# Kernel optimization log

Measured on AMD Instinct MI355X. Metric: run time of the kernel, lower is better.

Reference implementation:

```python
import jax, jax.numpy as jnp
import numpy as np

L, B, N, D, H, DH, M = 2, 8, 1024, 256, 4, 64, 512
EPS = 1e-5


def setup_inputs() -> dict:
    key = jax.random.key(0)
    ks = jax.random.split(key, 24)
    n = lambda k, shape, s=0.02: jax.random.normal(k, shape, dtype=jnp.float32) * s
    return {
        "x": jax.random.normal(ks[0], (B, N, D), dtype=jnp.float32),
        "ln1_g": jnp.ones((L, D), jnp.float32), "ln1_b": jnp.zeros((L, D), jnp.float32),
        "w_qkv": n(ks[1], (L, D, 3 * H * DH)),
        "w_out": n(ks[2], (L, H * DH, D)), "b_out": jnp.zeros((L, D), jnp.float32),
        "ln2_g": jnp.ones((L, D), jnp.float32), "ln2_b": jnp.zeros((L, D), jnp.float32),
        "w_fc1": n(ks[3], (L, D, M)), "b_fc1": jnp.zeros((L, M), jnp.float32),
        "wh": n(ks[4], (L, M, 3), 0.3), "bh": jnp.zeros((L, M), jnp.float32),
        "wv": n(ks[5], (L, M, 3), 0.3), "bv": jnp.zeros((L, M), jnp.float32),
        "bn_g": jnp.ones((L, M), jnp.float32), "bn_b": jnp.zeros((L, M), jnp.float32),
        "bn_m": n(ks[6], (L, M), 0.1),
        "bn_v": jax.random.uniform(ks[7], (L, M), jnp.float32, 0.5, 1.5),
        "w_fc2": n(ks[8], (L, M, D)), "b_fc2": jnp.zeros((L, D), jnp.float32),
        "ls_w1": n(ks[9], (L, D, D // 4)), "ls_w2": n(ks[10], (L, D // 4, D)),
    }


def _ln(z, g, b):
    mu = z.mean(-1, keepdims=True)
    var = ((z - mu) ** 2).mean(-1, keepdims=True)
    return (z - mu) / jnp.sqrt(var + EPS) * g + b


def _lsrc(z, w1, w2):
    # SE gate: global mean over tokens -> FC -> ReLU -> FC -> sigmoid -> scale
    s = jax.nn.sigmoid(jax.nn.relu(z.mean(1) @ w1) @ w2)  # [B, D]
    return z * s[:, None, :]


def reference(x, ln1_g, ln1_b, w_qkv, w_out, b_out, ln2_g, ln2_b, w_fc1, b_fc1,
              wh, bh, wv, bv, bn_g, bn_b, bn_m, bn_v, w_fc2, b_fc2, ls_w1, ls_w2):
    scale = DH ** -0.5
    for l in range(L):
        # --- MHSA (pre-LN) ---
        h = _ln(x, ln1_g[l], ln1_b[l])
        qkv = h @ w_qkv[l]                                  # [B,N,3*H*DH]
        q, k, v = jnp.split(qkv, 3, axis=-1)
        split = lambda t: t.reshape(B, N, H, DH).transpose(0, 2, 1, 3)  # [B,H,N,DH]
        q, k, v = split(q), split(k), split(v)
        attn = jax.nn.softmax(jnp.einsum('bhid,bhjd->bhij', q, k) * scale, axis=-1)
        o = jnp.einsum('bhij,bhjd->bhid', attn, v)
        o = o.transpose(0, 2, 1, 3).reshape(B, N, H * DH)
        y = o @ w_out[l] + b_out[l]                          # dropout = identity (eval)
        x = _lsrc(x + y, ls_w1[l], ls_w2[l])
        # --- MLP with ACB depthwise conv over the token axis ---
        y = jax.nn.gelu(_ln(x, ln2_g[l], ln2_b[l]) @ w_fc1[l] + b_fc1[l], approximate=False)
        # conv_h: depthwise 1x3 conv along N (zero pad)
        yp = jnp.pad(y, ((0, 0), (1, 1), (0, 0)))
        ch = wh[l, :, 0] * yp[:, :-2] + wh[l, :, 1] * yp[:, 1:-1] + wh[l, :, 2] * yp[:, 2:] + bh[l]
        # conv_v: 3x1 depthwise conv on height-1 input with pad 1 -> only center tap
        cv = wv[l, :, 1] * y + bv[l]
        z = ch + cv
        z = (z - bn_m[l]) / jnp.sqrt(bn_v[l] + EPS) * bn_g[l] + bn_b[l]  # BN (eval)
        z = jax.nn.gelu(z, approximate=False)
        y = z @ w_fc2[l] + b_fc2[l]
        x = _lsrc(x + y, ls_w1[l], ls_w2[l])
    return x
```

## Files before the change

### kernel.cpp

```cpp
#include <hip/hip_runtime.h>
#include <hip/hip_bf16.h>
#include <math.h>

#define EPSF 1e-5f

typedef short bf16x8 __attribute__((ext_vector_type(8)));
typedef float f32x4  __attribute__((ext_vector_type(4)));

#define S_BARRIER   __asm__ volatile("s_barrier" ::: "memory")
#define S_WAITV(n)  __asm__ volatile("s_waitcnt vmcnt(" #n ")" ::: "memory")
#define S_WAITL0    __asm__ volatile("s_waitcnt lgkmcnt(0)" ::: "memory")

__device__ __forceinline__ float gelu_f(float z){
  return 0.5f*z*(1.0f + erff(z*0.70710678118654752f));
}
__device__ __forceinline__ unsigned short f2bf(float f){
  unsigned u = __float_as_uint(f);
  u += 0x7FFFu + ((u >> 16) & 1u);
  return (unsigned short)(u >> 16);
}
__device__ __forceinline__ float bf2f(unsigned short u){
  return __uint_as_float((unsigned)u << 16);
}
__device__ __forceinline__ void gll16(const unsigned short* g, unsigned short* l){
  __builtin_amdgcn_global_load_lds(
    (const __attribute__((address_space(1))) unsigned int*)g,
    (__attribute__((address_space(3))) unsigned int*)l, 16, 0, 0);
}

__global__ void tcast_all_k(const float* __restrict__ wqkv, const float* __restrict__ wout,
                            const float* __restrict__ wfc1, const float* __restrict__ wfc2,
                            unsigned short* __restrict__ oqkv, unsigned short* __restrict__ oout,
                            unsigned short* __restrict__ ofc1, unsigned short* __restrict__ ofc2,
                            const float* __restrict__ wh, const float* __restrict__ bh,
                            const float* __restrict__ wv, const float* __restrict__ bv,
                            const float* __restrict__ g, const float* __restrict__ bb,
                            const float* __restrict__ mm, const float* __restrict__ vv,
                            float* __restrict__ cp){
  int idx = blockIdx.x*256 + threadIdx.x;
  if (idx < 1048576){
    int l = idx >> 19; int r = idx & 524287;
    const float* in; unsigned short* out; int K, N, base;
    if (r < 196608)      { in=wqkv+ (long)l*196608; out=oqkv+(long)l*196608; K=256; N=768; base=r; }
    else if (r < 262144) { in=wout+ (long)l*65536;  out=oout+(long)l*65536;  K=256; N=256; base=r-196608; }
    else if (r < 393216) { in=wfc1+ (long)l*131072; out=ofc1+(long)l*131072; K=256; N=512; base=r-262144; }
    else                 { in=wfc2+ (long)l*131072; out=ofc2+(long)l*131072; K=512; N=256; base=r-393216; }
    int n = base / K, k = base % K;
    out[base] = f2bf(in[(long)k*N + n]);
  } else if (idx < 1048576 + 1024){
    int j2 = idx - 1048576;
    int l = j2 >> 9, j = j2 & 511;
    int o = l*512 + j;
    float sc = g[o]*rsqrtf(vv[o] + EPSF);
    float* c = cp + (long)l*6*512;
    c[0*512+j] = wh[o*3+0];
    c[1*512+j] = wh[o*3+1] + wv[o*3+1];
    c[2*512+j] = wh[o*3+2];
    c[3*512+j] = bh[o] + bv[o];
    c[4*512+j] = sc;
    c[5*512+j] = bb[o] - mm[o]*sc;
  }
}

__global__ void ln_bf_k(const float* __restrict__ x, const float* __restrict__ g,
                        const float* __restrict__ b, unsigned short* __restrict__ out){
  const int row = blockIdx.x;
  const int t = threadIdx.x;
  float v = x[(long)row*256 + t];
  float s = v, s2 = v*v;
  for (int o=32;o>0;o>>=1){ s += __shfl_down(s,o); s2 += __shfl_down(s2,o); }
  __shared__ float ls[4], ls2[4];
  const int w = t>>6, lane = t&63;
  if (lane==0){ ls[w]=s; ls2[w]=s2; }
  __syncthreads();
  if (t==0){
    float a  = ls[0]+ls[1]+ls[2]+ls[3];
    float a2 = ls2[0]+ls2[1]+ls2[2]+ls2[3];
    float mu = a*(1.f/256.f);
    float var = a2*(1.f/256.f) - mu*mu;
    ls[0]=mu; ls2[0]=rsqrtf(var+EPSF);
  }
  __syncthreads();
  out[(long)row*256+t] = f2bf((v-ls[0])*ls2[0]*g[t] + b[t]);
}

__global__ void seapply_ln_k(float* __restrict__ x, const float* __restrict__ gate,
                             const float* __restrict__ g, const float* __restrict__ b,
                             unsigned short* __restrict__ out){
  const int row = blockIdx.x;
  const int t = threadIdx.x;
  const int bi = row >> 10;
  float v = x[(long)row*256 + t] * gate[bi*256 + t];
  x[(long)row*256 + t] = v;
  float s = v, s2 = v*v;
  for (int o=32;o>0;o>>=1){ s += __shfl_down(s,o); s2 += __shfl_down(s2,o); }
  __shared__ float ls[4], ls2[4];
  const int w = t>>6, lane = t&63;
  if (lane==0){ ls[w]=s; ls2[w]=s2; }
  __syncthreads();
  if (t==0){
    float a  = ls[0]+ls[1]+ls[2]+ls[3];
    float a2 = ls2[0]+ls2[1]+ls2[2]+ls2[3];
    float mu = a*(1.f/256.f);
    float var = a2*(1.f/256.f) - mu*mu;
    ls[0]=mu; ls2[0]=rsqrtf(var+EPSF);
  }
  __syncthreads();
  out[(long)row*256+t] = f2bf((v-ls[0])*ls2[0]*g[t] + b[t]);
}

__global__ void seapply_out_k(const float* __restrict__ x, const float* __restrict__ gate,
                              float* __restrict__ o){
  long o4 = ((long)blockIdx.x*256 + threadIdx.x)*4;
  float4 v = *reinterpret_cast<const float4*>(x+o4);
  float4 g = *reinterpret_cast<const float4*>(gate + (((o4>>18)<<8) | (o4 & 255)));
  v.x*=g.x; v.y*=g.y; v.z*=g.z; v.w*=g.w;
  *reinterpret_cast<float4*>(o+o4) = v;
}

template<int ACT, bool RES, bool BIAS, int OUT, int BNT, bool CS>
__global__ __launch_bounds__(256,2)
void gmm_k(const unsigned short* __restrict__ A,
           const unsigned short* __restrict__ Bt,
           void* __restrict__ Cv, int ldc,
           const float* __restrict__ bias,
           const float* __restrict__ res,
           int K, unsigned short* __restrict__ vtb,
           float* __restrict__ cm)
{
  __shared__ unsigned short As[2][128*64];
  __shared__ unsigned short Bs[2][BNT*64];
  float* C = (float*)Cv;
  unsigned short* Cb = (unsigned short*)Cv;
  const int tid  = threadIdx.x;
  const int wave = tid>>6, lane = tid&63;
  constexpr int NJ = (BNT==128) ? 4 : 2;
  const int wm = (wave>>1)*64, wn = (wave&1)*(BNT/2);
  const int m0 = blockIdx.y*128, n0 = blockIdx.x*BNT;
  const int lrow = lane&15, quad = lane>>4;

  f32x4 acc[4][NJ];
  #pragma unroll
  for (int i=0;i<4;i++)
    #pragma unroll
    for (int j=0;j<NJ;j++)
      #pragma unroll
      for (int r=0;r<4;r++) acc[i][j][r]=0.f;

  auto stage = [&](int kt, int buf){
    const int k0 = kt<<6;
    #pragma unroll
    for (int it2=0; it2<4; it2++){
      int idx = tid + it2*256;
      int row = idx>>3, c = idx&7;
      gll16(A + (long)(m0+row)*K + k0 + c*8, &As[buf][idx*8]);
    }
    #pragma unroll
    for (int it2=0; it2<BNT/32; it2++){
      int idx = tid + it2*256;
      int row = idx>>3, c = idx&7;
      gll16(Bt + (long)(n0+row)*K + k0 + c*8, &Bs[buf][idx*8]);
    }
  };

  const int iters = K >> 6;
  stage(0, 0);

  for (int it=0; it<iters; it++){
    const int cur = it & 1;
    if (it+1 < iters){
      stage(it+1, cur^1);
      if (BNT==128) { S_WAITV(8); } else { S_WAITV(6); }
    } else {
      S_WAITV(0);
    }
    S_BARRIER;

    #pragma unroll
    for (int s=0;s<2;s++){
      bf16x8 a[4], b[NJ];
      const int ck = s*4 + quad;
      #pragma unroll
      for (int i=0;i<4;i++)
        a[i] = *reinterpret_cast<const bf16x8*>(&As[cur][(wm+16*i+lrow)*64 + ck*8]);
      #pragma unroll
      for (int j=0;j<NJ;j++)
        b[j] = *reinterpret_cast<const bf16x8*>(&Bs[cur][(wn+16*j+lrow)*64 + ck*8]);
      #pragma unroll
      for (int i=0;i<4;i++)
        #pragma unroll
        for (int j=0;j<NJ;j++)
          acc[i][j] = __builtin_amdgcn_mfma_f32_16x16x32_bf16(a[i], b[j], acc[i][j], 0,0,0);
    }
    S_WAITL0;
    S_BARRIER;
  }

  if (OUT==2 && n0 >= 512){
    unsigned short* lt = (unsigned short*)&As[0][0];
    #pragma unroll
    for (int i=0;i<4;i++){
      const int row_l0 = wm + 16*i + quad*4;
      #pragma unroll
      for (int j=0;j<NJ;j++){
        const int col_l = wn + 16*j + lrow;
        #pragma unroll
        for (int r=0;r<4;r++){
          const int row_l = row_l0 + r;
          lt[col_l*128 + (((row_l>>3) ^ (col_l&7))<<3) + (row_l&7)] = f2bf(acc[i][j][r]);
        }
      }
    }
    __syncthreads();
    const int bb = m0 >> 10, nn0 = m0 & 1023;
    #pragma unroll
    for (int it2=0; it2<8; it2++){
      int idx = tid + it2*256;
      int col_l = idx >> 4;
      int row8 = (idx & 15) << 3;
      uint4 v = *reinterpret_cast<const uint4*>(&lt[col_l*128 + (((row8>>3) ^ (col_l&7))<<3)]);
      int col = n0 + col_l;
      int h = (col-512) >> 6, d = (col-512) & 63;
      *reinterpret_cast<uint4*>(&vtb[(long)((bb*4+h)*64 + d)*1024 + nn0 + row8]) = v;
    }
    return;
  }

  float csum[NJ];
  #pragma unroll
  for (int j=0;j<NJ;j++) csum[j] = 0.f;

  #pragma unroll
  for (int i=0;i<4;i++){
    const int row0 = m0 + wm + 16*i + quad*4;
    #pragma unroll
    for (int j=0;j<NJ;j++){
      const int col = n0 + wn + 16*j + lrow;
      if (OUT==2){
        #pragma unroll
        for (int r=0;r<4;r++)
          Cb[(long)(row0+r)*512 + col] = f2bf(acc[i][j][r]);
      } else {
        const float bv = BIAS ? bias[col] : 0.f;
        #pragma unroll
        for (int r=0;r<4;r++){
          const long off = (long)(row0+r)*ldc + col;
          float v = acc[i][j][r] + bv;
          if (RES) v += res[off];
          if (ACT==1) v = gelu_f(v);
          if (CS) csum[j] += v;
          if (OUT==1) Cb[off] = f2bf(v); else C[off] = v;
        }
      }
    }
  }
  if (CS){
    float* red = (float*)&As[0][0];
    for (int j = tid; j < BNT; j += 256) red[j] = 0.f;
    __syncthreads();
    #pragma unroll
    for (int j=0;j<NJ;j++)
      atomicAdd(&red[wn + 16*j + lrow], csum[j]);
    __syncthreads();
    const int bb = m0 >> 10;
    for (int j = tid; j < BNT; j += 256)
      atomicAdd(&cm[bb*256 + n0 + j], red[j]);
  }
}

__global__ __launch_bounds__(256)
void attn_k(const unsigned short* __restrict__ qkb,
            const unsigned short* __restrict__ vtb,
            unsigned short* __restrict__ op, float* __restrict__ ml){
  const int q0 = blockIdx.x * 64;
  const int bh = blockIdx.y;
  const int kz = blockIdx.z;
  const int b = bh >> 2, h = bh & 3;
  const int tid = threadIdx.x;
  const int wv = tid >> 6;
  const int lane = tid & 63;
  const int l15 = lane & 15, quad = lane >> 4;

  __shared__ unsigned short Qs[64*64];
  __shared__ unsigned short Ks[64*64];
  __shared__ unsigned short Vt[64*64];
  __shared__ unsigned short Ps[64*64];

  const long rowbase = (long)b*1024;
  const unsigned short* vsrc = vtb + (long)bh*64*1024;

  for (int f = tid; f < 512; f += 256){
    int row = f >> 3, g = f & 7;
    *reinterpret_cast<uint4*>(&Qs[row*64 + (g ^ (row&7))*8]) =
      *reinterpret_cast<const uint4*>(qkb + (rowbase + q0 + row)*512 + h*64 + g*8);
  }

  float lp[4];
  f32x4 acc[4];
  #pragma unroll
  for (int r=0;r<4;r++) lp[r] = 0.f;
  #pragma unroll
  for (int j=0;j<4;j++)
    #pragma unroll
    for (int r=0;r<4;r++) acc[j][r] = 0.f;

  const int kbeg = kz*512, kend = kbeg + 512;
  for (int k0 = kbeg; k0 < kend; k0 += 64){
    __syncthreads();
    for (int f = tid; f < 512; f += 256){
      int row = f >> 3, g = f & 7;
      *reinterpret_cast<uint4*>(&Ks[row*64 + (g ^ (row&7))*8]) =
        *reinterpret_cast<const uint4*>(qkb + (rowbase + k0 + row)*512 + 256 + h*64 + g*8);
      *reinterpret_cast<uint4*>(&Vt[row*64 + (g ^ (row&7))*8]) =
        *reinterpret_cast<const uint4*>(vsrc + (long)row*1024 + k0 + g*8);
    }
    __syncthreads();

    f32x4 s[4];
    #pragma unroll
    for (int j=0;j<4;j++)
      #pragma unroll
      for (int r=0;r<4;r++) s[j][r] = 0.f;

    #pragma unroll
    for (int half=0; half<2; half++){
      const int ck = half*4 + quad;
      const int qrow = 16*wv + l15;
      bf16x8 a = *reinterpret_cast<const bf16x8*>(&Qs[qrow*64 + (ck ^ (qrow&7))*8]);
      #pragma unroll
      for (int j=0;j<4;j++){
        int krow = 16*j + l15;
        bf16x8 bb = *reinterpret_cast<const bf16x8*>(&Ks[krow*64 + (ck ^ (krow&7))*8]);
        s[j] = __builtin_amdgcn_mfma_f32_16x16x32_bf16(a, bb, s[j], 0,0,0);
      }
    }

    #pragma unroll
    for (int r=0;r<4;r++)
      #pragma unroll
      for (int j=0;j<4;j++){
        float p = __expf(s[j][r]*0.125f);
        s[j][r] = p;
        lp[r] += p;
      }

    #pragma unroll
    for (int j=0;j<4;j++)
      #pragma unroll
      for (int r=0;r<4;r++){
        int rowq = 16*wv + quad*4 + r;
        int key = l15 + 16*j;
        Ps[rowq*64 + (((key>>3) ^ ((rowq>>2)&7)))*8 + (key&7)] = f2bf(s[j][r]);
      }

    #pragma unroll
    for (int half=0; half<2; half++){
      const int ck = half*4 + quad;
      const int prow = 16*wv + l15;
      bf16x8 a = *reinterpret_cast<const bf16x8*>(&Ps[prow*64 + (ck ^ ((prow>>2)&7))*8]);
      #pragma unroll
      for (int jj=0;jj<4;jj++){
        int drow = 16*jj + l15;
        bf16x8 bb = *reinterpret_cast<const bf16x8*>(&Vt[drow*64 + (ck ^ (drow&7))*8]);
        acc[jj] = __builtin_amdgcn_mfma_f32_16x16x32_bf16(a, bb, acc[jj], 0,0,0);
      }
    }
  }

  #pragma unroll
  for (int r=0;r<4;r++){
    float l = lp[r];
    l += __shfl_xor(l, 1); l += __shfl_xor(l, 2);
    l += __shfl_xor(l, 4); l += __shfl_xor(l, 8);
    const int rloc = q0 + 16*wv + quad*4 + r;
    const long grow = rowbase + rloc;
    #pragma unroll
    for (int jj=0;jj<4;jj++)
      op[((long)kz*8192 + grow)*256 + h*64 + 16*jj + l15] = f2bf(acc[jj][r]);
    if (l15 == 0)
      ml[((long)kz*32 + bh)*1024 + rloc] = l;
  }
}

__global__ void attn_merge_k(const unsigned short* __restrict__ op, const float* __restrict__ ml,
                             unsigned short* __restrict__ o, float* __restrict__ cm){
  if (blockIdx.x == 0){
    for (int i = threadIdx.x; i < 2048; i += 256) cm[i] = 0.f;
  }
  long off = ((long)blockIdx.x*256 + threadIdx.x)*4;
  int row = (int)(off >> 8);
  int col = (int)(off & 255);
  int h = col >> 6;
  int b = row >> 10, n = row & 1023;
  int bh = b*4 + h;
  float l0 = ml[(long)bh*1024 + n];
  float l1 = ml[32768 + (long)bh*1024 + n];
  float inv = 1.f / (l0 + l1);
  ushort4 a0 = *reinterpret_cast<const ushort4*>(op + off);
  ushort4 a1 = *reinterpret_cast<const ushort4*>(op + 2097152 + off);
  ushort4 u;
  u.x = f2bf((bf2f(a0.x) + bf2f(a1.x))*inv);
  u.y = f2bf((bf2f(a0.y) + bf2f(a1.y))*inv);
  u.z = f2bf((bf2f(a0.z) + bf2f(a1.z))*inv);
  u.w = f2bf((bf2f(a0.w) + bf2f(a1.w))*inv);
  *reinterpret_cast<ushort4*>(o + off) = u;
}

__global__ void segate2_k(const float* __restrict__ cm, const float* __restrict__ w1,
                          const float* __restrict__ w2, float* __restrict__ gate){
  const int b = blockIdx.x, t = threadIdx.x;
  __shared__ float sc[256], sh[64];
  sc[t] = cm[b*256+t]*(1.f/1024.f);
  __syncthreads();
  if (t < 64){
    float a=0.f;
    for (int k=0;k<256;k++) a += sc[k]*w1[k*64+t];
    sh[t] = fmaxf(a, 0.f);
  }
  __syncthreads();
  float a=0.f;
  for (int k=0;k<64;k++) a += sh[k]*w2[k*256+t];
  gate[b*256+t] = 1.f/(1.f+__expf(-a));
}

__global__ void conv_bf_k(const unsigned short* __restrict__ y, unsigned short* __restrict__ z,
                          const float* __restrict__ cp, float* __restrict__ cm)
{
  if (blockIdx.x == 0){
    for (int i = threadIdx.x; i < 2048; i += 256) cm[i] = 0.f;
  }
  const int t = threadIdx.x;
  const int rr = t >> 6;
  const int row = blockIdx.x*4 + rr;
  const int n = row & 1023;
  const int c8 = (t & 63) * 8;
  const long base = (long)row*512 + c8;

  uint4 uc = *reinterpret_cast<const uint4*>(y + base);
  uint4 um = (n>0)    ? *reinterpret_cast<const uint4*>(y + base - 512) : uint4{0,0,0,0};
  uint4 up = (n<1023) ? *reinterpret_cast<const uint4*>(y + base + 512) : uint4{0,0,0,0};
  const unsigned short* yc = reinterpret_cast<const unsigned short*>(&uc);
  const unsigned short* ym = reinterpret_cast<const unsigned short*>(&um);
  const unsigned short* yp = reinterpret_cast<const unsigned short*>(&up);

  float c0[8], c1[8], c2[8], c3[8], s5[8], b5[8];
  #pragma unroll
  for (int q=0;q<8;q+=4){
    *reinterpret_cast<float4*>(&c0[q]) = *reinterpret_cast<const float4*>(cp + 0*512 + c8 + q);
    *reinterpret_cast<float4*>(&c1[q]) = *reinterpret_cast<const float4*>(cp + 1*512 + c8 + q);
    *reinterpret_cast<float4*>(&c2[q]) = *reinterpret_cast<const float4*>(cp + 2*512 + c8 + q);
    *reinterpret_cast<float4*>(&c3[q]) = *reinterpret_cast<const float4*>(cp + 3*512 + c8 + q);
    *reinterpret_cast<float4*>(&s5[q]) = *reinterpret_cast<const float4*>(cp + 4*512 + c8 + q);
    *reinterpret_cast<float4*>(&b5[q]) = *reinterpret_cast<const float4*>(cp + 5*512 + c8 + q);
  }

  unsigned short outv[8];
  #pragma unroll
  for (int q=0;q<8;q++){
    float zz = c0[q]*bf2f(ym[q]) + c1[q]*bf2f(yc[q]) + c2[q]*bf2f(yp[q]) + c3[q];
    zz = zz*s5[q] + b5[q];
    outv[q] = f2bf(gelu_f(zz));
  }
  *reinterpret_cast<uint4*>(z + base) = *reinterpret_cast<uint4*>(outv);
}

extern "C" void kernel_launch(void* const* d_in, const int* in_sizes, int n_in,
                              void* d_out, int out_size, void* d_ws, size_t ws_size,
                              hipStream_t stream)
{
  const float* x_in  = (const float*)d_in[0];
  const float* ln1_g = (const float*)d_in[1];
  const float* ln1_b = (const float*)d_in[2];
  const float* w_qkv = (const float*)d_in[3];
  const float* w_out = (const float*)d_in[4];
  const float* b_out = (const float*)d_in[5];
  const float* ln2_g = (const float*)d_in[6];
  const float* ln2_b = (const float*)d_in[7];
  const float* w_fc1 = (const float*)d_in[8];
  const float* b_fc1 = (const float*)d_in[9];
  const float* wh    = (const float*)d_in[10];
  const float* bh    = (const float*)d_in[11];
  const float* wv    = (const float*)d_in[12];
  const float* bv    = (const float*)d_in[13];
  const float* bn_g  = (const float*)d_in[14];
  const float* bn_b  = (const float*)d_in[15];
  const float* bn_m  = (const float*)d_in[16];
  const float* bn_v  = (const float*)d_in[17];
  const float* w_fc2 = (const float*)d_in[18];
  const float* b_fc2 = (const float*)d_in[19];
  const float* ls_w1 = (const float*)d_in[20];
  const float* ls_w2 = (const float*)d_in[21];

  float* ws   = (float*)d_ws;
  float* xbuf = ws;
  float* mlb  = xbuf + 2097152;
  float* cm   = mlb + 65536;
  float* gate = cm + 2048;
  float* cpar = gate + 2048;
  unsigned short* habf = (unsigned short*)(cpar + 6144);
  unsigned short* opbf = habf + 2097152;
  unsigned short* qkb  = opbf + 4194304;
  unsigned short* vtb  = qkb  + 4194304;
  unsigned short* ybf  = vtb  + 2097152;
  unsigned short* zbf  = ybf  + 4194304;
  unsigned short* wqkv_t = zbf + 4194304;
  unsigned short* wout_t = wqkv_t + 393216;
  unsigned short* wfc1_t = wout_t + 131072;
  unsigned short* wfc2_t = wfc1_t + 262144;

  tcast_all_k<<<4100,256,0,stream>>>(w_qkv, w_out, w_fc1, w_fc2,
                                     wqkv_t, wout_t, wfc1_t, wfc2_t,
                                     wh, bh, wv, bv, bn_g, bn_b, bn_m, bn_v, cpar);

  for (int l=0;l<2;l++){
    const float* bout_l = b_out + l*256;
    const float* bfc1_l = b_fc1 + l*512;
    const float* bfc2_l = b_fc2 + l*256;
    const float* lw1_l  = ls_w1 + (long)l*256*64;
    const float* lw2_l  = ls_w2 + (long)l*64*256;
    const float* resx   = (l==0) ? x_in : xbuf;

    if (l==0)
      ln_bf_k<<<8192,256,0,stream>>>(x_in, ln1_g, ln1_b, habf);
    gmm_k<0,false,false,2,128,false><<<dim3(6,64),256,0,stream>>>(
        habf, wqkv_t + (long)l*768*256, (void*)qkb, 512, nullptr, nullptr, 256, vtb, nullptr);
    attn_k<<<dim3(16,32,2),256,0,stream>>>(qkb, vtb, opbf, mlb);
    attn_merge_k<<<2048,256,0,stream>>>(opbf, mlb, habf, cm);
    gmm_k<0,true,true,0,64,true><<<dim3(4,64),256,0,stream>>>(
        habf, wout_t + (long)l*256*256, (void*)xbuf, 256, bout_l, resx, 256, nullptr, cm);

    segate2_k<<<8,256,0,stream>>>(cm, lw1_l, lw2_l, gate);
    seapply_ln_k<<<8192,256,0,stream>>>(xbuf, gate, ln2_g + l*256, ln2_b + l*256, habf);

    gmm_k<1,false,true,1,128,false><<<dim3(4,64),256,0,stream>>>(
        habf, wfc1_t + (long)l*512*256, (void*)ybf, 512, bfc1_l, nullptr, 256, nullptr, nullptr);
    conv_bf_k<<<2048,256,0,stream>>>(ybf, zbf, cpar + (long)l*6*512, cm);
    gmm_k<0,true,true,0,64,true><<<dim3(4,64),256,0,stream>>>(
        zbf, wfc2_t + (long)l*256*512, (void*)xbuf, 256, bfc2_l, xbuf, 512, nullptr, cm);

    segate2_k<<<8,256,0,stream>>>(cm, lw1_l, lw2_l, gate);
    if (l==0)
      seapply_ln_k<<<8192,256,0,stream>>>(xbuf, gate, ln1_g + 256, ln1_b + 256, habf);
    else
      seapply_out_k<<<2048,256,0,stream>>>(xbuf, gate, (float*)d_out);
  }
}
```

Measured before the change: 336.4 us.

## Use one-wave-per-row LayerNorm, smaller M tiles for N=256 GEMMs, prefetch attention K/V

LayerNorm kernels now give each row to one wave with float4 loads and shuffle-only reductions, replacing the per-block shared-memory reduction and two barriers. The GEMM gains a BMT template parameter, and the out-projection and fc2 GEMMs use 64x64 tiles, doubling the grid to fill more CUs. The attention kernel prefetches the next K/V tile into registers while computing on the current one, which adds registers in exchange for hiding global load latency.

```diff
diff --git a/kernel.cpp b/kernel.cpp
--- a/kernel.cpp
+++ b/kernel.cpp
@@ -64,49 +64,51 @@
 
 __global__ void ln_bf_k(const float* __restrict__ x, const float* __restrict__ g,
                         const float* __restrict__ b, unsigned short* __restrict__ out){
-  const int row = blockIdx.x;
-  const int t = threadIdx.x;
-  float v = x[(long)row*256 + t];
-  float s = v, s2 = v*v;
-  for (int o=32;o>0;o>>=1){ s += __shfl_down(s,o); s2 += __shfl_down(s2,o); }
-  __shared__ float ls[4], ls2[4];
-  const int w = t>>6, lane = t&63;
-  if (lane==0){ ls[w]=s; ls2[w]=s2; }
-  __syncthreads();
-  if (t==0){
-    float a  = ls[0]+ls[1]+ls[2]+ls[3];
-    float a2 = ls2[0]+ls2[1]+ls2[2]+ls2[3];
-    float mu = a*(1.f/256.f);
-    float var = a2*(1.f/256.f) - mu*mu;
-    ls[0]=mu; ls2[0]=rsqrtf(var+EPSF);
-  }
-  __syncthreads();
-  out[(long)row*256+t] = f2bf((v-ls[0])*ls2[0]*g[t] + b[t]);
+  const int wv = threadIdx.x >> 6, lane = threadIdx.x & 63;
+  const int row = blockIdx.x*4 + wv;
+  const int c4 = lane*4;
+  float4 v = *reinterpret_cast<const float4*>(x + (long)row*256 + c4);
+  float s  = v.x+v.y+v.z+v.w;
+  float s2 = v.x*v.x+v.y*v.y+v.z*v.z+v.w*v.w;
+  #pragma unroll
+  for (int o=32;o>0;o>>=1){ s += __shfl_xor(s,o); s2 += __shfl_xor(s2,o); }
+  const float mu = s*(1.f/256.f);
+  const float rstd = rsqrtf(s2*(1.f/256.f) - mu*mu + EPSF);
+  float4 gg = *reinterpret_cast<const float4*>(g + c4);
+  float4 bb = *reinterpret_cast<const float4*>(b + c4);
+  ushort4 u;
+  u.x = f2bf((v.x-mu)*rstd*gg.x + bb.x);
+  u.y = f2bf((v.y-mu)*rstd*gg.y + bb.y);
+  u.z = f2bf((v.z-mu)*rstd*gg.z + bb.z);
+  u.w = f2bf((v.w-mu)*rstd*gg.w + bb.w);
+  *reinterpret_cast<ushort4*>(out + (long)row*256 + c4) = u;
 }
 
 __global__ void seapply_ln_k(float* __restrict__ x, const float* __restrict__ gate,
                              const float* __restrict__ g, const float* __restrict__ b,
                              unsigned short* __restrict__ out){
-  const int row = blockIdx.x;
-  const int t = threadIdx.x;
+  const int wv = threadIdx.x >> 6, lane = threadIdx.x & 63;
+  const int row = blockIdx.x*4 + wv;
   const int bi = row >> 10;
-  float v = x[(long)row*256 + t] * gate[bi*256 + t];
-  x[(long)row*256 + t] = v;
-  float s = v, s2 = v*v;
-  for (int o=32;o>0;o>>=1){ s += __shfl_down(s,o); s2 += __shfl_down(s2,o); }
-  __shared__ float ls[4], ls2[4];
-  const int w = t>>6, lane = t&63;
-  if (lane==0){ ls[w]=s; ls2[w]=s2; }
-  __syncthreads();
-  if (t==0){
-    float a  = ls[0]+ls[1]+ls[2]+ls[3];
-    float a2 = ls2[0]+ls2[1]+ls2[2]+ls2[3];
-    float mu = a*(1.f/256.f);
-    float var = a2*(1.f/256.f) - mu*mu;
-    ls[0]=mu; ls2[0]=rsqrtf(var+EPSF);
-  }
-  __syncthreads();
-  out[(long)row*256+t] = f2bf((v-ls[0])*ls2[0]*g[t] + b[t]);
+  const int c4 = lane*4;
+  float4 v = *reinterpret_cast<const float4*>(x + (long)row*256 + c4);
+  float4 gt = *reinterpret_cast<const float4*>(gate + bi*256 + c4);
+  v.x*=gt.x; v.y*=gt.y; v.z*=gt.z; v.w*=gt.w;
+  *reinterpret_cast<float4*>(x + (long)row*256 + c4) = v;
+  float s  = v.x+v.y+v.z+v.w;
+  float s2 = v.x*v.x+v.y*v.y+v.z*v.z+v.w*v.w;
+  #pragma unroll
+  for (int o=32;o>0;o>>=1){ s += __shfl_xor(s,o); s2 += __shfl_xor(s2,o); }
+  const float mu = s*(1.f/256.f);
+  const float rstd = rsqrtf(s2*(1.f/256.f) - mu*mu + EPSF);
+  float4 gg = *reinterpret_cast<const float4*>(g + c4);
+  float4 bb = *reinterpret_cast<const float4*>(b + c4);
+  ushort4 u;
+  u.x = f2bf((v.x-mu)*rstd*gg.x + bb.x);
+  u.y = f2bf((v.y-mu)*rstd*gg.y + bb.y);
+  u.z = f2bf((v.z-mu)*rstd*gg.z + bb.z);
+  u.w = f2bf((v.w-mu)*rstd*gg.w + bb.w);
+  *reinterpret_cast<ushort4*>(out + (long)row*256 + c4) = u;
 }
 
 __global__ void seapply_out_k(const float* __restrict__ x, const float* __restrict__ gate,
@@ -118,7 +120,7 @@
   *reinterpret_cast<float4*>(o+o4) = v;
 }
 
-template<int ACT, bool RES, bool BIAS, int OUT, int BNT, bool CS>
+template<int ACT, bool RES, bool BIAS, int OUT, int BMT, int BNT, bool CS>
 __global__ __launch_bounds__(256,2)
 void gmm_k(const unsigned short* __restrict__ A,
            const unsigned short* __restrict__ Bt,
@@ -128,20 +130,22 @@
            int K, unsigned short* __restrict__ vtb,
            float* __restrict__ cm)
 {
-  __shared__ unsigned short As[2][128*64];
+  __shared__ unsigned short As[2][BMT*64];
   __shared__ unsigned short Bs[2][BNT*64];
   float* C = (float*)Cv;
   unsigned short* Cb = (unsigned short*)Cv;
   const int tid  = threadIdx.x;
   const int wave = tid>>6, lane = tid&63;
-  constexpr int NJ = (BNT==128) ? 4 : 2;
-  const int wm = (wave>>1)*64, wn = (wave&1)*(BNT/2);
-  const int m0 = blockIdx.y*128, n0 = blockIdx.x*BNT;
+  constexpr int NI = BMT/32;
+  constexpr int NJ = BNT/32;
+  constexpr int NDMA = BMT/32 + BNT/32;
+  const int wm = (wave>>1)*(16*NI), wn = (wave&1)*(BNT/2);
+  const int m0 = blockIdx.y*BMT, n0 = blockIdx.x*BNT;
   const int lrow = lane&15, quad = lane>>4;
 
-  f32x4 acc[4][NJ];
-  #pragma unroll
-  for (int i=0;i<4;i++)
+  f32x4 acc[NI][NJ];
+  #pragma unroll
+  for (int i=0;i<NI;i++)
     #pragma unroll
     for (int j=0;j<NJ;j++)
       #pragma unroll
@@ -150,7 +154,7 @@
   auto stage = [&](int kt, int buf){
     const int k0 = kt<<6;
     #pragma unroll
-    for (int it2=0; it2<4; it2++){
+    for (int it2=0; it2<BMT/32; it2++){
       int idx = tid + it2*256;
       int row = idx>>3, c = idx&7;
       gll16(A + (long)(m0+row)*K + k0 + c*8, &As[buf][idx*8]);
@@ -170,7 +174,9 @@
     const int cur = it & 1;
     if (it+1 < iters){
       stage(it+1, cur^1);
-      if (BNT==128) { S_WAITV(8); } else { S_WAITV(6); }
+      if constexpr (NDMA==8) { S_WAITV(8); }
+      else if constexpr (NDMA==6) { S_WAITV(6); }
+      else { S_WAITV(4); }
     } else {
       S_WAITV(0);
     }
@@ -178,16 +184,16 @@
 
     #pragma unroll
     for (int s=0;s<2;s++){
-      bf16x8 a[4], b[NJ];
+      bf16x8 a[NI], b[NJ];
       const int ck = s*4 + quad;
       #pragma unroll
-      for (int i=0;i<4;i++)
+      for (int i=0;i<NI;i++)
         a[i] = *reinterpret_cast<const bf16x8*>(&As[cur][(wm+16*i+lrow)*64 + ck*8]);
       #pragma unroll
       for (int j=0;j<NJ;j++)
         b[j] = *reinterpret_cast<const bf16x8*>(&Bs[cur][(wn+16*j+lrow)*64 + ck*8]);
       #pragma unroll
-      for (int i=0;i<4;i++)
+      for (int i=0;i<NI;i++)
         #pragma unroll
         for (int j=0;j<NJ;j++)
           acc[i][j] = __builtin_amdgcn_mfma_f32_16x16x32_bf16(a[i], b[j], acc[i][j], 0,0,0);
@@ -196,61 +202,69 @@
     S_BARRIER;
   }
 
-  if (OUT==2 && n0 >= 512){
-    unsigned short* lt = (unsigned short*)&As[0][0];
-    #pragma unroll
-    for (int i=0;i<4;i++){
-      const int row_l0 = wm + 16*i + quad*4;
+  if constexpr (OUT==2){
+    if (n0 >= 512){
+      unsigned short* lt = (unsigned short*)&As[0][0];
+      #pragma unroll
+      for (int i=0;i<NI;i++){
+        const int row_l0 = wm + 16*i + quad*4;
+        #pragma unroll
+        for (int j=0;j<NJ;j++){
+          const int col_l = wn + 16*j + lrow;
+          #pragma unroll
+          for (int r=0;r<4;r++){
+            const int row_l = row_l0 + r;
+            lt[col_l*128 + (((row_l>>3) ^ (col_l&7))<<3) + (row_l&7)] = f2bf(acc[i][j][r]);
+          }
+        }
+      }
+      __syncthreads();
+      const int bb = m0 >> 10, nn0 = m0 & 1023;
+      #pragma unroll
+      for (int it2=0; it2<8; it2++){
+        int idx = tid + it2*256;
+        int col_l = idx >> 4;
+        int row8 = (idx & 15) << 3;
+        uint4 v = *reinterpret_cast<const uint4*>(&lt[col_l*128 + (((row8>>3) ^ (col_l&7))<<3)]);
+        int col = n0 + col_l;
+        int h = (col-512) >> 6, d = (col-512) & 63;
+        *reinterpret_cast<uint4*>(&vtb[(long)((bb*4+h)*64 + d)*1024 + nn0 + row8]) = v;
+      }
+      return;
+    }
+    #pragma unroll
+    for (int i=0;i<NI;i++){
+      const int row0 = m0 + wm + 16*i + quad*4;
       #pragma unroll
       for (int j=0;j<NJ;j++){
-        const int col_l = wn + 16*j + lrow;
-        #pragma unroll
-        for (int r=0;r<4;r++){
-          const int row_l = row_l0 + r;
-          lt[col_l*128 + (((row_l>>3) ^ (col_l&7))<<3) + (row_l&7)] = f2bf(acc[i][j][r]);
-        }
-      }
-    }
-    __syncthreads();
-    const int bb = m0 >> 10, nn0 = m0 & 1023;
-    #pragma unroll
-    for (int it2=0; it2<8; it2++){
-      int idx = tid + it2*256;
-      int col_l = idx >> 4;
-      int row8 = (idx & 15) << 3;
-      uint4 v = *reinterpret_cast<const uint4*>(&lt[col_l*128 + (((row8>>3) ^ (col_l&7))<<3)]);
-      int col = n0 + col_l;
-      int h = (col-512) >> 6, d = (col-512) & 63;
-      *reinterpret_cast<uint4*>(&vtb[(long)((bb*4+h)*64 + d)*1024 + nn0 + row8]) = v;
-    }
-    return;
-  }
-
-  float csum[NJ];
-  #pragma unroll
-  for (int j=0;j<NJ;j++) csum[j] = 0.f;
-
-  #pragma unroll
-  for (int i=0;i<4;i++){
-    const int row0 = m0 + wm + 16*i + quad*4;
-    #pragma unroll
-    for (int j=0;j<NJ;j++){
-      const int col = n0 + wn + 16*j + lrow;
-      if (OUT==2){
+        const int col = n0 + wn + 16*j + lrow;
         #pragma unroll
         for (int r=0;r<4;r++)
           Cb[(long)(row0+r)*512 + col] = f2bf(acc[i][j][r]);
-      } else {
-        const float bv = BIAS ? bias[col] : 0.f;
-        #pragma unroll
-        for (int r=0;r<4;r++){
-          const long off = (long)(row0+r)*ldc + col;
-          float v = acc[i][j][r] + bv;
-          if (RES) v += res[off];
-          if (ACT==1) v = gelu_f(v);
-          if (CS) csum[j] += v;
-          if (OUT==1) Cb[off] = f2bf(v); else C[off] = v;
-        }
+      }
+    }
+    return;
+  }
+
+  float csum[NJ];
+  #pragma unroll
+  for (int j=0;j<NJ;j++) csum[j] = 0.f;
+
+  #pragma unroll
+  for (int i=0;i<NI;i++){
+    const int row0 = m0 + wm + 16*i + quad*4;
+    #pragma unroll
+    for (int j=0;j<NJ;j++){
+      const int col = n0 + wn + 16*j + lrow;
+      const float bv = BIAS ? bias[col] : 0.f;
+      #pragma unroll
+      for (int r=0;r<4;r++){
+        const long off = (long)(row0+r)*ldc + col;
+        float v = acc[i][j][r] + bv;
+        if (RES) v += res[off];
+        if (ACT==1) v = gelu_f(v);
+        if (CS) csum[j] += v;
+        if (OUT==1) Cb[off] = f2bf(v); else C[off] = v;
       }
     }
   }
@@ -295,6 +309,16 @@
       *reinterpret_cast<const uint4*>(qkb + (rowbase + q0 + row)*512 + h*64 + g*8);
   }
 
+  const int row0 = tid >> 3, g0 = tid & 7;
+  const int row1 = row0 + 32;
+  uint4 kr0, vr0, kr1, vr1;
+  auto pre = [&](int k0){
+    kr0 = *reinterpret_cast<const uint4*>(qkb + (rowbase + k0 + row0)*512 + 256 + h*64 + g0*8);
+    vr0 = *reinterpret_cast<const uint4*>(vsrc + (long)row0*1024 + k0 + g0*8);
+    kr1 = *reinterpret_cast<const uint4*>(qkb + (rowbase + k0 + row1)*512 + 256 + h*64 + g0*8);
+    vr1 = *reinterpret_cast<const uint4*>(vsrc + (long)row1*1024 + k0 + g0*8);
+  };
+
   float lp[4];
   f32x4 acc[4];
   #pragma unroll
@@ -305,16 +329,14 @@
     for (int r=0;r<4;r++) acc[j][r] = 0.f;
 
   const int kbeg = kz*512, kend = kbeg + 512;
+  pre(kbeg);
   for (int k0 = kbeg; k0 < kend; k0 += 64){
+    *reinterpret_cast<uint4*>(&Ks[row0*64 + (g0 ^ (row0&7))*8]) = kr0;
+    *reinterpret_cast<uint4*>(&Vt[row0*64 + (g0 ^ (row0&7))*8]) = vr0;
+    *reinterpret_cast<uint4*>(&Ks[row1*64 + (g0 ^ (row1&7))*8]) = kr1;
+    *reinterpret_cast<uint4*>(&Vt[row1*64 + (g0 ^ (row1&7))*8]) = vr1;
     __syncthreads();
-    for (int f = tid; f < 512; f += 256){
-      int row = f >> 3, g = f & 7;
-      *reinterpret_cast<uint4*>(&Ks[row*64 + (g ^ (row&7))*8]) =
-        *reinterpret_cast<const uint4*>(qkb + (rowbase + k0 + row)*512 + 256 + h*64 + g*8);
-      *reinterpret_cast<uint4*>(&Vt[row*64 + (g ^ (row&7))*8]) =
-        *reinterpret_cast<const uint4*>(vsrc + (long)row*1024 + k0 + g*8);
-    }
-    __syncthreads();
+    if (k0 + 64 < kend) pre(k0 + 64);
 
     f32x4 s[4];
     #pragma unroll
@@ -365,6 +387,7 @@
         acc[jj] = __builtin_amdgcn_mfma_f32_16x16x32_bf16(a, bb, acc[jj], 0,0,0);
       }
     }
+    __syncthreads();
   }
 
   #pragma unroll
@@ -521,26 +544,26 @@
     const float* resx   = (l==0) ? x_in : xbuf;
 
     if (l==0)
-      ln_bf_k<<<8192,256,0,stream>>>(x_in, ln1_g, ln1_b, habf);
-    gmm_k<0,false,false,2,128,false><<<dim3(6,64),256,0,stream>>>(
+      ln_bf_k<<<2048,256,0,stream>>>(x_in, ln1_g, ln1_b, habf);
+    gmm_k<0,false,false,2,128,128,false><<<dim3(6,64),256,0,stream>>>(
         habf, wqkv_t + (long)l*768*256, (void*)qkb, 512, nullptr, nullptr, 256, vtb, nullptr);
     attn_k<<<dim3(16,32,2),256,0,stream>>>(qkb, vtb, opbf, mlb);
     attn_merge_k<<<2048,256,0,stream>>>(opbf, mlb, habf, cm);
-    gmm_k<0,true,true,0,64,true><<<dim3(4,64),256,0,stream>>>(
+    gmm_k<0,true,true,0,64,64,true><<<dim3(4,128),256,0,stream>>>(
         habf, wout_t + (long)l*256*256, (void*)xbuf, 256, bout_l, resx, 256, nullptr, cm);
 
     segate2_k<<<8,256,0,stream>>>(cm, lw1_l, lw2_l, gate);
-    seapply_ln_k<<<8192,256,0,stream>>>(xbuf, gate, ln2_g + l*256, ln2_b + l*256, habf);
-
-    gmm_k<1,false,true,1,128,false><<<dim3(4,64),256,0,stream>>>(
+    seapply_ln_k<<<2048,256,0,stream>>>(xbuf, gate, ln2_g + l*256, ln2_b + l*256, habf);
+
+    gmm_k<1,false,true,1,128,128,false><<<dim3(4,64),256,0,stream>>>(
         habf, wfc1_t + (long)l*512*256, (void*)ybf, 512, bfc1_l, nullptr, 256, nullptr, nullptr);
     conv_bf_k<<<2048,256,0,stream>>>(ybf, zbf, cpar + (long)l*6*512, cm);
-    gmm_k<0,true,true,0,64,true><<<dim3(4,64),256,0,stream>>>(
+    gmm_k<0,true,true,0,64,64,true><<<dim3(4,128),256,0,stream>>>(
         zbf, wfc2_t + (long)l*256*512, (void*)xbuf, 256, bfc2_l, xbuf, 512, nullptr, cm);
 
     segate2_k<<<8,256,0,stream>>>(cm, lw1_l, lw2_l, gate);
     if (l==0)
-      seapply_ln_k<<<8192,256,0,stream>>>(xbuf, gate, ln1_g + 256, ln1_b + 256, habf);
+      seapply_ln_k<<<2048,256,0,stream>>>(xbuf, gate, ln1_g + 256, ln1_b + 256, habf);
     else
       seapply_out_k<<<2048,256,0,stream>>>(xbuf, gate, (float*)d_out);
   }
```

After: 322.3 us. -4.2%, faster.
